# Optimization experiments

Hardware: AMD Instinct MI355X
Metric: run time of the kernel (lower is better)

Reference implementation:

```python
import jax, jax.numpy as jnp
import numpy as np

DT = 0.1
TAU_MIN = 1.0
TAU_MAX = 10.0
LN_EPS = 1e-5


def setup_inputs() -> dict:
    key = jax.random.key(0)
    ks = jax.random.split(key, 8)
    B, S, I, H = 64, 1024, 256, 512
    s_in = 1.0 / np.sqrt(I)
    s_rec = 1.0 / np.sqrt(H)
    s_tau1 = 1.0 / np.sqrt(I + H)
    s_tau2 = 1.0 / np.sqrt(H)
    return {
        "x": jax.random.normal(ks[0], (B, S, I), dtype=jnp.float32),
        "h0": jnp.zeros((B, H), dtype=jnp.float32),
        "W_in": jax.random.uniform(ks[1], (H, I), jnp.float32, -s_in, s_in),
        "b_in": jax.random.uniform(ks[2], (H,), jnp.float32, -s_in, s_in),
        "W_rec": jax.random.uniform(ks[3], (H, H), jnp.float32, -s_rec, s_rec),
        "tau_w1": jax.random.uniform(ks[4], (H, I + H), jnp.float32, -s_tau1, s_tau1),
        "tau_b1": jax.random.uniform(ks[5], (H,), jnp.float32, -s_tau1, s_tau1),
        "tau_w2": jax.random.uniform(ks[6], (1, H), jnp.float32, -s_tau2, s_tau2),
        "tau_b2": jax.random.uniform(ks[7], (1,), jnp.float32, -s_tau2, s_tau2),
        "gamma": jnp.ones((H,), dtype=jnp.float32),
        "beta": jnp.zeros((H,), dtype=jnp.float32),
    }


def _layernorm(h, gamma, beta):
    mu = jnp.mean(h, axis=-1, keepdims=True)
    var = jnp.mean(jnp.square(h - mu), axis=-1, keepdims=True)
    return (h - mu) * jax.lax.rsqrt(var + LN_EPS) * gamma + beta


def reference(x, h0, W_in, b_in, W_rec, tau_w1, tau_b1, tau_w2, tau_b2, gamma, beta):
    # x: [B, S, I] -> scan over time with carry h: [B, H]
    def step(h, x_t):
        combined = jnp.concatenate([x_t, h], axis=-1)                     # [B, I+H]
        t_hid = jnp.tanh(combined @ tau_w1.T + tau_b1)                    # [B, H]
        tau_raw = jax.nn.sigmoid(t_hid @ tau_w2.T + tau_b2)               # [B, 1]
        tau = TAU_MIN + (TAU_MAX - TAU_MIN) * tau_raw                     # [B, 1]
        f_xh = jnp.tanh(x_t @ W_in.T + b_in + h @ W_rec.T)                # [B, H]
        h_new = h + DT * (-h + f_xh) / tau
        h_new = _layernorm(h_new, gamma, beta)
        return h_new, (h_new, tau)

    xs = jnp.swapaxes(x, 0, 1)                                            # [S, B, I]
    h_final, (outs, taus) = jax.lax.scan(step, h0, xs)
    output = jnp.swapaxes(outs, 0, 1)                                     # [B, S, H]
    tau_history = jnp.swapaxes(taus, 0, 1)                                # [B, S, 1]
    return output, h_final, tau_history
```

## Files before the change

### kernel.cpp

```cpp
#include <hip/hip_runtime.h>

#define S_LEN 1024
#define BATCH 64
#define I_DIM 256
#define H_DIM 512
#define NCL 4
#define NRK 32
#define ROWS 16
#define FPW 16
#define HSTR 520
#define XSTR 264

typedef short short8 __attribute__((ext_vector_type(8)));
typedef float floatx4 __attribute__((ext_vector_type(4)));
typedef unsigned short ushortx4 __attribute__((ext_vector_type(4)));

__device__ inline unsigned short f2bf(float x){
  unsigned u = __float_as_uint(x);
  u += 0x7fffu + ((u >> 16) & 1u);
  return (unsigned short)(u >> 16);
}
__device__ inline float bf2f(unsigned short s){
  return __uint_as_float(((unsigned)s) << 16);
}
__device__ inline float fast_tanh(float x){
  float e = __expf(2.0f * x);
  return 1.0f - 2.0f / (e + 1.0f);
}
__device__ inline float fast_sigmoid(float x){
  return 1.0f / (1.0f + __expf(-x));
}
__device__ inline short8 cvt8(const float* p){
  short8 r;
#pragma unroll
  for (int j = 0; j < 8; j++) r[j] = (short)f2bf(p[j]);
  return r;
}

__global__ __launch_bounds__(256) void convert_weights_kernel(
  const float* __restrict__ W_in, const float* __restrict__ tau_w1,
  unsigned short* __restrict__ Wbf, unsigned short* __restrict__ Tbf)
{
  const int f = blockIdx.x, k = threadIdx.x;
  Wbf[f * I_DIM + k] = f2bf(W_in[(size_t)f * I_DIM + k]);
  Tbf[f * I_DIM + k] = f2bf(tau_w1[(size_t)f * (I_DIM + H_DIM) + k]);
}

__global__ __launch_bounds__(256) void precompute_kernel(
  const float* __restrict__ x, const unsigned short* __restrict__ Wbf,
  const unsigned short* __restrict__ Tbf,
  const float* __restrict__ b_in, const float* __restrict__ tau_b1,
  unsigned short* __restrict__ A_in, unsigned short* __restrict__ A_tau)
{
  __shared__ unsigned short xs[BATCH * XSTR];
  const int t = blockIdx.x, tid = threadIdx.x;

  {
    const int br = tid >> 2, pp = tid & 3;
    const float* xrow = x + ((size_t)br * S_LEN + t) * I_DIM + pp * 64;
    unsigned short* drow = xs + br * XSTR + pp * 64;
#pragma unroll
    for (int c = 0; c < 16; c++){
      float4 v = *(const float4*)(xrow + c * 4);
      ushortx4 o; o[0] = f2bf(v.x); o[1] = f2bf(v.y); o[2] = f2bf(v.z); o[3] = f2bf(v.w);
      *(ushortx4*)(drow + c * 4) = o;
    }
  }
  __syncthreads();

  const int w = tid >> 6, l15 = tid & 15, q = (tid & 63) >> 4;
#pragma unroll 1
  for (int fb = 0; fb < 8; fb++){
    const int F = fb * 64 + w * 16 + l15;
    floatx4 accf[4], acct[4];
#pragma unroll
    for (int m = 0; m < 4; m++){ accf[m] = (floatx4){0,0,0,0}; acct[m] = (floatx4){0,0,0,0}; }
#pragma unroll
    for (int kc = 0; kc < 8; kc++){
      const int k0 = kc * 32 + q * 8;
      short8 bw = *(const short8*)&Wbf[F * I_DIM + k0];
      short8 bt = *(const short8*)&Tbf[F * I_DIM + k0];
#pragma unroll
      for (int m = 0; m < 4; m++){
        short8 a = *(const short8*)&xs[(m * 16 + l15) * XSTR + k0];
        accf[m] = __builtin_amdgcn_mfma_f32_16x16x32_bf16(a, bw, accf[m], 0, 0, 0);
        acct[m] = __builtin_amdgcn_mfma_f32_16x16x32_bf16(a, bt, acct[m], 0, 0, 0);
      }
    }
    const float bi = b_in[F], bt1 = tau_b1[F];
#pragma unroll
    for (int m = 0; m < 4; m++){
      ushortx4 pf, pt;
#pragma unroll
      for (int i2 = 0; i2 < 4; i2++){ pf[i2] = f2bf(accf[m][i2] + bi); pt[i2] = f2bf(acct[m][i2] + bt1); }
      const size_t base = ((size_t)t * H_DIM + F) * BATCH + m * 16 + q * 4;
      *(ushortx4*)(A_in + base) = pf;
      *(ushortx4*)(A_tau + base) = pt;
    }
  }
}

__global__ __launch_bounds__(256) void scan_kernel(
  const float* __restrict__ h0, const float* __restrict__ W_rec,
  const float* __restrict__ tau_w1, const float* __restrict__ tau_w2,
  const float* __restrict__ tau_b2_p, const float* __restrict__ gamma,
  const float* __restrict__ beta,
  const unsigned short* __restrict__ A_in, const unsigned short* __restrict__ A_tau,
  unsigned short* __restrict__ bc_f, float* __restrict__ bc_td,
  unsigned int* __restrict__ flags,
  float* __restrict__ out0, float* __restrict__ outh, float* __restrict__ outtau)
{
  __shared__ unsigned short hB[ROWS * HSTR];
  __shared__ float redf[4 * 64 * 9];

  const int tid = threadIdx.x;
  const int cl   = blockIdx.x & (NCL - 1);
  const int rank = blockIdx.x >> 2;
  const int w = tid >> 6, l64 = tid & 63, l15 = tid & 15, q = (tid & 63) >> 4;
  const int F0 = rank * FPW;
  const int i_id = tid >> 6;
  const int rb = ((l64 >> 4) << 2) + i_id;
  const int fl = l64 & 15;
  const int rr = tid >> 4;
  const int cc = tid & 15;

  short8 wr[4], wt[4];
#pragma unroll
  for (int c = 0; c < 4; c++){
    const int k = w * 128 + c * 32 + q * 8;
    wr[c] = cvt8(&W_rec[(size_t)(F0 + l15) * H_DIM + k]);
    wt[c] = cvt8(&tau_w1[(size_t)(F0 + l15) * (I_DIM + H_DIM) + I_DIM + k]);
  }
  float h_reg[32], gamr[32], betr[32];
  {
    const int b = cl * ROWS + rr;
#pragma unroll
    for (int j = 0; j < 32; j++){
      float hv = h0[(size_t)b * H_DIM + cc * 32 + j];
      h_reg[j] = hv;
      hB[rr * HSTR + cc * 32 + j] = f2bf(hv);
      gamr[j] = gamma[cc * 32 + j];
      betr[j] = beta[cc * 32 + j];
    }
  }
  const float tw2v = tau_w2[F0 + fl];
  const float tb2 = tau_b2_p[0];

  unsigned short af_raw, at_raw;
  {
    const size_t aidx = ((size_t)(F0 + fl)) * BATCH + cl * ROWS + rb;
    af_raw = A_in[aidx];
    at_raw = A_tau[aidx];
  }
  __syncthreads();

  for (int t = 0; t < S_LEN; t++){
    const float a_f = bf2f(af_raw);
    const float a_t = bf2f(at_raw);

    floatx4 af = {0,0,0,0}, at4 = {0,0,0,0};
#pragma unroll
    for (int c = 0; c < 4; c++){
      short8 ha = *(const short8*)&hB[l15 * HSTR + w * 128 + c * 32 + q * 8];
      af  = __builtin_amdgcn_mfma_f32_16x16x32_bf16(ha, wr[c], af,  0, 0, 0);
      at4 = __builtin_amdgcn_mfma_f32_16x16x32_bf16(ha, wt[c], at4, 0, 0, 0);
    }
    const int rbase = w * 576 + l64 * 9;
#pragma unroll
    for (int i2 = 0; i2 < 4; i2++){ redf[rbase + i2] = af[i2]; redf[rbase + 4 + i2] = at4[i2]; }
    __syncthreads();
    float vf = a_f, vt = a_t;
#pragma unroll
    for (int w2 = 0; w2 < 4; w2++){
      vf += redf[w2 * 576 + l64 * 9 + i_id];
      vt += redf[w2 * 576 + l64 * 9 + 4 + i_id];
    }
    vf = fast_tanh(vf);
    vt = fast_tanh(vt);

    const int par = t & 1;
    {
      unsigned pv = (unsigned)f2bf(vf);
      unsigned ov = (unsigned)__shfl_xor((int)pv, 1);
      if ((fl & 1) == 0){
        const size_t bcbase = ((size_t)(par * NCL + cl) * ROWS + rb) * H_DIM + F0 + fl;
        __hip_atomic_store((unsigned*)(bc_f + bcbase), pv | (ov << 16),
                           __ATOMIC_RELAXED, __HIP_MEMORY_SCOPE_AGENT);
      }
    }
    float pd = vt * tw2v;
    pd += __shfl_xor(pd, 1); pd += __shfl_xor(pd, 2);
    pd += __shfl_xor(pd, 4); pd += __shfl_xor(pd, 8);
    if (fl == 0)
      __hip_atomic_store(&bc_td[((size_t)(par * NCL + cl) * NRK + rank) * ROWS + rb], pd,
                         __ATOMIC_RELAXED, __HIP_MEMORY_SCOPE_AGENT);

    __builtin_amdgcn_s_waitcnt(0);
    __syncthreads();
    const int fbi = (par * NCL + cl) << 5;
    if (tid == 0)
      __hip_atomic_store(&flags[fbi | rank], (unsigned)(t + 1),
                         __ATOMIC_RELAXED, __HIP_MEMORY_SCOPE_AGENT);
    if (t + 1 < S_LEN){
      const size_t aidx = ((size_t)(t + 1) * H_DIM + (F0 + fl)) * BATCH + cl * ROWS + rb;
      af_raw = A_in[aidx];
      at_raw = A_tau[aidx];
    }
    if (w == 0){
      const unsigned tgt = (unsigned)(t + 1);
      while (__hip_atomic_load(&flags[fbi | (l64 & 31)],
                               __ATOMIC_RELAXED, __HIP_MEMORY_SCOPE_AGENT) < tgt)
        __builtin_amdgcn_s_sleep(1);
    }
    asm volatile("" ::: "memory");
    __syncthreads();

    float fv[32];
    const size_t fbase = ((size_t)(par * NCL + cl) * ROWS + rr) * H_DIM + cc * 32;
#pragma unroll
    for (int u = 0; u < 8; u++){
      unsigned long long v = __hip_atomic_load((const unsigned long long*)(bc_f + fbase + u * 4),
                                               __ATOMIC_RELAXED, __HIP_MEMORY_SCOPE_AGENT);
#pragma unroll
      for (int e = 0; e < 4; e++) fv[u * 4 + e] = bf2f((unsigned short)(v >> (16 * e)));
    }
    float td = __hip_atomic_load(&bc_td[((size_t)(par * NCL + cl) * NRK + cc) * ROWS + rr],
                                 __ATOMIC_RELAXED, __HIP_MEMORY_SCOPE_AGENT)
             + __hip_atomic_load(&bc_td[((size_t)(par * NCL + cl) * NRK + cc + 16) * ROWS + rr],
                                 __ATOMIC_RELAXED, __HIP_MEMORY_SCOPE_AGENT);
    td += __shfl_xor(td, 1); td += __shfl_xor(td, 2);
    td += __shfl_xor(td, 4); td += __shfl_xor(td, 8);
    const float tau = 1.0f + 9.0f * fast_sigmoid(td + tb2);
    const float c2 = 0.1f / tau, c1 = 1.0f - c2;

    float hp[32]; float s1 = 0.f, s2 = 0.f;
#pragma unroll
    for (int j = 0; j < 32; j++){
      float v2 = c1 * h_reg[j] + c2 * fv[j];
      hp[j] = v2; s1 += v2; s2 += v2 * v2;
    }
    s1 += __shfl_xor(s1, 1); s2 += __shfl_xor(s2, 1);
    s1 += __shfl_xor(s1, 2); s2 += __shfl_xor(s2, 2);
    s1 += __shfl_xor(s1, 4); s2 += __shfl_xor(s2, 4);
    s1 += __shfl_xor(s1, 8); s2 += __shfl_xor(s2, 8);
    const float mu = s1 * (1.0f / 512.0f);
    const float var = s2 * (1.0f / 512.0f) - mu * mu;
    const float rs = rsqrtf(var + 1e-5f);
#pragma unroll
    for (int j = 0; j < 32; j++) h_reg[j] = (hp[j] - mu) * rs * gamr[j] + betr[j];

#pragma unroll
    for (int u = 0; u < 4; u++){
      short8 hv;
#pragma unroll
      for (int e = 0; e < 8; e++) hv[e] = (short)f2bf(h_reg[u * 8 + e]);
      *(short8*)&hB[rr * HSTR + cc * 32 + u * 8] = hv;
    }
    if (cc == (rank >> 1)){
      const int j0 = (rank & 1) * 16;
      float* dst = out0 + ((size_t)(cl * ROWS + rr) * S_LEN + t) * H_DIM + rank * FPW;
#pragma unroll
      for (int j2 = 0; j2 < 16; j2++) dst[j2] = h_reg[j0 + j2];
    }
    if (rank == 0 && cc == 0) outtau[(size_t)(cl * ROWS + rr) * S_LEN + t] = tau;
    if (t == S_LEN - 1 && rank == 0){
#pragma unroll
      for (int j = 0; j < 32; j++)
        outh[(size_t)(cl * ROWS + rr) * H_DIM + cc * 32 + j] = h_reg[j];
    }
    __syncthreads();
  }
}

extern "C" void kernel_launch(void* const* d_in, const int* in_sizes, int n_in,
                              void* d_out, int out_size, void* d_ws, size_t ws_size,
                              hipStream_t stream) {
  const float* x      = (const float*)d_in[0];
  const float* h0     = (const float*)d_in[1];
  const float* W_in   = (const float*)d_in[2];
  const float* b_in   = (const float*)d_in[3];
  const float* W_rec  = (const float*)d_in[4];
  const float* tau_w1 = (const float*)d_in[5];
  const float* tau_b1 = (const float*)d_in[6];
  const float* tau_w2 = (const float*)d_in[7];
  const float* tau_b2 = (const float*)d_in[8];
  const float* gamma  = (const float*)d_in[9];
  const float* beta   = (const float*)d_in[10];

  char* ws = (char*)d_ws;
  unsigned short* A_in   = (unsigned short*)(ws);
  unsigned short* A_tau  = (unsigned short*)(ws + 67108864);
  unsigned short* bc_f   = (unsigned short*)(ws + 134217728);
  float*          bc_td  = (float*)(ws + 134348800);
  unsigned int*   flags  = (unsigned int*)(ws + 134365184);
  unsigned short* Wbf    = (unsigned short*)(ws + 134366208);
  unsigned short* Tbf    = (unsigned short*)(ws + 134628352);

  float* out0   = (float*)d_out;
  float* outh   = out0 + (size_t)BATCH * S_LEN * H_DIM;
  float* outtau = outh + (size_t)BATCH * H_DIM;

  hipMemsetAsync(flags, 0, 1024, stream);
  convert_weights_kernel<<<dim3(H_DIM), 256, 0, stream>>>(W_in, tau_w1, Wbf, Tbf);
  precompute_kernel<<<dim3(S_LEN), 256, 0, stream>>>(x, Wbf, Tbf, b_in, tau_b1, A_in, A_tau);
  scan_kernel<<<dim3(NCL * NRK), 256, 0, stream>>>(h0, W_rec, tau_w1, tau_w2, tau_b2, gamma, beta,
                                                   A_in, A_tau, bc_f, bc_td, flags,
                                                   out0, outh, outtau);
}
```

Baseline: 4.455 ms.

## Embed step tags in exchanged data, drop flag barrier, use fewer wider scan blocks

The scan now runs 32 blocks (8 ranks per cluster) instead of 128. Each wave owns 16 features over the full K=512, which removes the LDS cross-wave reduction and one __syncthreads per step. The separate flag array and its spin/barrier are replaced by stamping the step index into each exchanged bf16 value and tau partial, so consumers poll only for the exact data they need. The exchange buffers reuse the weight-conversion scratch space. The trade-off is fewer CUs, more MFMAs per wave, a larger register footprint for the weights, and per-element polling of global memory.

```diff
diff --git a/kernel.cpp b/kernel.cpp
--- a/kernel.cpp
+++ b/kernel.cpp
@@ -5,15 +5,15 @@
 #define I_DIM 256
 #define H_DIM 512
 #define NCL 4
-#define NRK 32
+#define NRK 8
 #define ROWS 16
-#define FPW 16
 #define HSTR 520
 #define XSTR 264
 
 typedef short short8 __attribute__((ext_vector_type(8)));
 typedef float floatx4 __attribute__((ext_vector_type(4)));
 typedef unsigned short ushortx4 __attribute__((ext_vector_type(4)));
+typedef unsigned long long u64;
 
 __device__ inline unsigned short f2bf(float x){
   unsigned u = __float_as_uint(x);
@@ -54,7 +54,6 @@
 {
   __shared__ unsigned short xs[BATCH * XSTR];
   const int t = blockIdx.x, tid = threadIdx.x;
-
   {
     const int br = tid >> 2, pp = tid & 3;
     const float* xrow = x + ((size_t)br * S_LEN + t) * I_DIM + pp * 64;
@@ -100,36 +99,31 @@
   }
 }
 
-__global__ __launch_bounds__(256) void scan_kernel(
+__global__ __launch_bounds__(256, 1) void scan_kernel(
   const float* __restrict__ h0, const float* __restrict__ W_rec,
   const float* __restrict__ tau_w1, const float* __restrict__ tau_w2,
   const float* __restrict__ tau_b2_p, const float* __restrict__ gamma,
   const float* __restrict__ beta,
   const unsigned short* __restrict__ A_in, const unsigned short* __restrict__ A_tau,
-  unsigned short* __restrict__ bc_f, float* __restrict__ bc_td,
-  unsigned int* __restrict__ flags,
+  unsigned* __restrict__ bc_f, u64* __restrict__ bc_td,
   float* __restrict__ out0, float* __restrict__ outh, float* __restrict__ outtau)
 {
   __shared__ unsigned short hB[ROWS * HSTR];
-  __shared__ float redf[4 * 64 * 9];
 
   const int tid = threadIdx.x;
   const int cl   = blockIdx.x & (NCL - 1);
   const int rank = blockIdx.x >> 2;
-  const int w = tid >> 6, l64 = tid & 63, l15 = tid & 15, q = (tid & 63) >> 4;
-  const int F0 = rank * FPW;
-  const int i_id = tid >> 6;
-  const int rb = ((l64 >> 4) << 2) + i_id;
-  const int fl = l64 & 15;
+  const int w = tid >> 6, l15 = tid & 15, q = (tid & 63) >> 4;
+  const int Fw = rank * 64 + w * 16 + l15;
   const int rr = tid >> 4;
   const int cc = tid & 15;
 
-  short8 wr[4], wt[4];
-#pragma unroll
-  for (int c = 0; c < 4; c++){
-    const int k = w * 128 + c * 32 + q * 8;
-    wr[c] = cvt8(&W_rec[(size_t)(F0 + l15) * H_DIM + k]);
-    wt[c] = cvt8(&tau_w1[(size_t)(F0 + l15) * (I_DIM + H_DIM) + I_DIM + k]);
+  short8 wr[16], wt[16];
+#pragma unroll
+  for (int kc = 0; kc < 16; kc++){
+    const int k = kc * 32 + q * 8;
+    wr[kc] = cvt8(&W_rec[(size_t)Fw * H_DIM + k]);
+    wt[kc] = cvt8(&tau_w1[(size_t)Fw * (I_DIM + H_DIM) + I_DIM + k]);
   }
   float h_reg[32], gamr[32], betr[32];
   {
@@ -143,91 +137,92 @@
       betr[j] = beta[cc * 32 + j];
     }
   }
-  const float tw2v = tau_w2[F0 + fl];
+  const float tw2v = tau_w2[Fw];
   const float tb2 = tau_b2_p[0];
 
-  unsigned short af_raw, at_raw;
+  ushortx4 afp, atp;
   {
-    const size_t aidx = ((size_t)(F0 + fl)) * BATCH + cl * ROWS + rb;
-    af_raw = A_in[aidx];
-    at_raw = A_tau[aidx];
+    const size_t aidx = (size_t)Fw * BATCH + cl * ROWS + q * 4;
+    afp = *(const ushortx4*)(A_in + aidx);
+    atp = *(const ushortx4*)(A_tau + aidx);
   }
   __syncthreads();
 
   for (int t = 0; t < S_LEN; t++){
-    const float a_f = bf2f(af_raw);
-    const float a_t = bf2f(at_raw);
-
-    floatx4 af = {0,0,0,0}, at4 = {0,0,0,0};
-#pragma unroll
-    for (int c = 0; c < 4; c++){
-      short8 ha = *(const short8*)&hB[l15 * HSTR + w * 128 + c * 32 + q * 8];
-      af  = __builtin_amdgcn_mfma_f32_16x16x32_bf16(ha, wr[c], af,  0, 0, 0);
-      at4 = __builtin_amdgcn_mfma_f32_16x16x32_bf16(ha, wt[c], at4, 0, 0, 0);
-    }
-    const int rbase = w * 576 + l64 * 9;
-#pragma unroll
-    for (int i2 = 0; i2 < 4; i2++){ redf[rbase + i2] = af[i2]; redf[rbase + 4 + i2] = at4[i2]; }
+    const unsigned st = (unsigned)(t + 1);
+    const int par = t & 1;
+    const int pc16 = (par * NCL + cl) * ROWS;
+
+    floatx4 Df = {0,0,0,0}, Dt = {0,0,0,0};
+#pragma unroll
+    for (int kc = 0; kc < 16; kc++){
+      short8 ha = *(const short8*)&hB[l15 * HSTR + kc * 32 + q * 8];
+      Df = __builtin_amdgcn_mfma_f32_16x16x32_bf16(ha, wr[kc], Df, 0, 0, 0);
+      Dt = __builtin_amdgcn_mfma_f32_16x16x32_bf16(ha, wt[kc], Dt, 0, 0, 0);
+    }
+    float pd[4];
+#pragma unroll
+    for (int i = 0; i < 4; i++){
+      float vf = fast_tanh(Df[i] + bf2f(afp[i]));
+      float vt = fast_tanh(Dt[i] + bf2f(atp[i]));
+      __hip_atomic_store(&bc_f[(size_t)(pc16 + q * 4 + i) * H_DIM + Fw],
+                         (unsigned)f2bf(vf) | (st << 16),
+                         __ATOMIC_RELAXED, __HIP_MEMORY_SCOPE_AGENT);
+      pd[i] = vt * tw2v;
+    }
+#pragma unroll
+    for (int i = 0; i < 4; i++){
+      pd[i] += __shfl_xor(pd[i], 1); pd[i] += __shfl_xor(pd[i], 2);
+      pd[i] += __shfl_xor(pd[i], 4); pd[i] += __shfl_xor(pd[i], 8);
+    }
+    if (l15 == 0){
+#pragma unroll
+      for (int i = 0; i < 4; i++)
+        __hip_atomic_store(&bc_td[(size_t)(pc16 + q * 4 + i) * 32 + rank * 4 + w],
+                           (u64)__float_as_uint(pd[i]) | ((u64)st << 32),
+                           __ATOMIC_RELAXED, __HIP_MEMORY_SCOPE_AGENT);
+    }
+    if (t + 1 < S_LEN){
+      const size_t aidx = ((size_t)(t + 1) * H_DIM + Fw) * BATCH + cl * ROWS + q * 4;
+      afp = *(const ushortx4*)(A_in + aidx);
+      atp = *(const ushortx4*)(A_tau + aidx);
+    }
     __syncthreads();
-    float vf = a_f, vt = a_t;
-#pragma unroll
-    for (int w2 = 0; w2 < 4; w2++){
-      vf += redf[w2 * 576 + l64 * 9 + i_id];
-      vt += redf[w2 * 576 + l64 * 9 + 4 + i_id];
-    }
-    vf = fast_tanh(vf);
-    vt = fast_tanh(vt);
-
-    const int par = t & 1;
-    {
-      unsigned pv = (unsigned)f2bf(vf);
-      unsigned ov = (unsigned)__shfl_xor((int)pv, 1);
-      if ((fl & 1) == 0){
-        const size_t bcbase = ((size_t)(par * NCL + cl) * ROWS + rb) * H_DIM + F0 + fl;
-        __hip_atomic_store((unsigned*)(bc_f + bcbase), pv | (ov << 16),
-                           __ATOMIC_RELAXED, __HIP_MEMORY_SCOPE_AGENT);
+
+    const u64* fsrc = (const u64*)&bc_f[(size_t)(pc16 + rr) * H_DIM + cc * 32];
+    u64 tmp[16];
+#pragma unroll
+    for (int u = 0; u < 16; u++)
+      tmp[u] = __hip_atomic_load(&fsrc[u], __ATOMIC_RELAXED, __HIP_MEMORY_SCOPE_AGENT);
+    unsigned pend = 0;
+#pragma unroll
+    for (int u = 0; u < 16; u++){
+      unsigned s0 = (unsigned)(tmp[u] >> 16) & 0xFFFFu;
+      unsigned s1 = (unsigned)(tmp[u] >> 48);
+      if (s0 != st || s1 != st) pend |= 1u << u;
+    }
+    while (pend){
+#pragma unroll
+      for (int u = 0; u < 16; u++) if (pend & (1u << u)){
+        u64 v = __hip_atomic_load(&fsrc[u], __ATOMIC_RELAXED, __HIP_MEMORY_SCOPE_AGENT);
+        unsigned s0 = (unsigned)(v >> 16) & 0xFFFFu;
+        unsigned s1 = (unsigned)(v >> 48);
+        if (s0 == st && s1 == st){ tmp[u] = v; pend &= ~(1u << u); }
       }
     }
-    float pd = vt * tw2v;
-    pd += __shfl_xor(pd, 1); pd += __shfl_xor(pd, 2);
-    pd += __shfl_xor(pd, 4); pd += __shfl_xor(pd, 8);
-    if (fl == 0)
-      __hip_atomic_store(&bc_td[((size_t)(par * NCL + cl) * NRK + rank) * ROWS + rb], pd,
-                         __ATOMIC_RELAXED, __HIP_MEMORY_SCOPE_AGENT);
-
-    __builtin_amdgcn_s_waitcnt(0);
-    __syncthreads();
-    const int fbi = (par * NCL + cl) << 5;
-    if (tid == 0)
-      __hip_atomic_store(&flags[fbi | rank], (unsigned)(t + 1),
-                         __ATOMIC_RELAXED, __HIP_MEMORY_SCOPE_AGENT);
-    if (t + 1 < S_LEN){
-      const size_t aidx = ((size_t)(t + 1) * H_DIM + (F0 + fl)) * BATCH + cl * ROWS + rb;
-      af_raw = A_in[aidx];
-      at_raw = A_tau[aidx];
-    }
-    if (w == 0){
-      const unsigned tgt = (unsigned)(t + 1);
-      while (__hip_atomic_load(&flags[fbi | (l64 & 31)],
-                               __ATOMIC_RELAXED, __HIP_MEMORY_SCOPE_AGENT) < tgt)
-        __builtin_amdgcn_s_sleep(1);
-    }
-    asm volatile("" ::: "memory");
-    __syncthreads();
-
     float fv[32];
-    const size_t fbase = ((size_t)(par * NCL + cl) * ROWS + rr) * H_DIM + cc * 32;
-#pragma unroll
-    for (int u = 0; u < 8; u++){
-      unsigned long long v = __hip_atomic_load((const unsigned long long*)(bc_f + fbase + u * 4),
-                                               __ATOMIC_RELAXED, __HIP_MEMORY_SCOPE_AGENT);
-#pragma unroll
-      for (int e = 0; e < 4; e++) fv[u * 4 + e] = bf2f((unsigned short)(v >> (16 * e)));
-    }
-    float td = __hip_atomic_load(&bc_td[((size_t)(par * NCL + cl) * NRK + cc) * ROWS + rr],
-                                 __ATOMIC_RELAXED, __HIP_MEMORY_SCOPE_AGENT)
-             + __hip_atomic_load(&bc_td[((size_t)(par * NCL + cl) * NRK + cc + 16) * ROWS + rr],
-                                 __ATOMIC_RELAXED, __HIP_MEMORY_SCOPE_AGENT);
+#pragma unroll
+    for (int u = 0; u < 16; u++){
+      fv[2 * u]     = bf2f((unsigned short)(tmp[u] & 0xFFFFu));
+      fv[2 * u + 1] = bf2f((unsigned short)((tmp[u] >> 32) & 0xFFFFu));
+    }
+    const u64* tsrc = &bc_td[(size_t)(pc16 + rr) * 32];
+    u64 t0, t1;
+    do { t0 = __hip_atomic_load(&tsrc[cc], __ATOMIC_RELAXED, __HIP_MEMORY_SCOPE_AGENT); }
+    while ((unsigned)(t0 >> 32) != st);
+    do { t1 = __hip_atomic_load(&tsrc[cc + 16], __ATOMIC_RELAXED, __HIP_MEMORY_SCOPE_AGENT); }
+    while ((unsigned)(t1 >> 32) != st);
+    float td = __uint_as_float((unsigned)t0) + __uint_as_float((unsigned)t1);
     td += __shfl_xor(td, 1); td += __shfl_xor(td, 2);
     td += __shfl_xor(td, 4); td += __shfl_xor(td, 8);
     const float tau = 1.0f + 9.0f * fast_sigmoid(td + tb2);
@@ -256,11 +251,10 @@
       for (int e = 0; e < 8; e++) hv[e] = (short)f2bf(h_reg[u * 8 + e]);
       *(short8*)&hB[rr * HSTR + cc * 32 + u * 8] = hv;
     }
-    if (cc == (rank >> 1)){
-      const int j0 = (rank & 1) * 16;
-      float* dst = out0 + ((size_t)(cl * ROWS + rr) * S_LEN + t) * H_DIM + rank * FPW;
-#pragma unroll
-      for (int j2 = 0; j2 < 16; j2++) dst[j2] = h_reg[j0 + j2];
+    if ((cc >> 1) == rank){
+      float* dst = out0 + ((size_t)(cl * ROWS + rr) * S_LEN + t) * H_DIM + cc * 32;
+#pragma unroll
+      for (int u = 0; u < 8; u++) *(float4*)(dst + u * 4) = *(float4*)(h_reg + u * 4);
     }
     if (rank == 0 && cc == 0) outtau[(size_t)(cl * ROWS + rr) * S_LEN + t] = tau;
     if (t == S_LEN - 1 && rank == 0){
@@ -288,22 +282,21 @@
   const float* beta   = (const float*)d_in[10];
 
   char* ws = (char*)d_ws;
-  unsigned short* A_in   = (unsigned short*)(ws);
-  unsigned short* A_tau  = (unsigned short*)(ws + 67108864);
-  unsigned short* bc_f   = (unsigned short*)(ws + 134217728);
-  float*          bc_td  = (float*)(ws + 134348800);
-  unsigned int*   flags  = (unsigned int*)(ws + 134365184);
-  unsigned short* Wbf    = (unsigned short*)(ws + 134366208);
-  unsigned short* Tbf    = (unsigned short*)(ws + 134628352);
+  unsigned short* A_in  = (unsigned short*)(ws);
+  unsigned short* A_tau = (unsigned short*)(ws + 67108864);
+  char* scratch = ws + 134217728;
+  unsigned short* Wbf  = (unsigned short*)(scratch);
+  unsigned short* Tbf  = (unsigned short*)(scratch + 262144);
+  unsigned*       bc_f = (unsigned*)(scratch);
+  u64*            bc_td= (u64*)(scratch + 262144);
 
   float* out0   = (float*)d_out;
   float* outh   = out0 + (size_t)BATCH * S_LEN * H_DIM;
   float* outtau = outh + (size_t)BATCH * H_DIM;
 
-  hipMemsetAsync(flags, 0, 1024, stream);
   convert_weights_kernel<<<dim3(H_DIM), 256, 0, stream>>>(W_in, tau_w1, Wbf, Tbf);
   precompute_kernel<<<dim3(S_LEN), 256, 0, stream>>>(x, Wbf, Tbf, b_in, tau_b1, A_in, A_tau);
   scan_kernel<<<dim3(NCL * NRK), 256, 0, stream>>>(h0, W_rec, tau_w1, tau_w2, tau_b2, gamma, beta,
-                                                   A_in, A_tau, bc_f, bc_td, flags,
+                                                   A_in, A_tau, bc_f, bc_td,
                                                    out0, outh, outtau);
 }
```

Result: slower. 5.909 ms (+32.6%).
